# Performance work log

Hardware: AMD Instinct MI355X
Metric: run time of the kernel (lower is better)

Reference implementation:

```python
import jax, jax.numpy as jnp
import numpy as np
import math

FEATURE_DIM = 192  # per-axis dim = 64, n_freqs per axis = 32


def setup_inputs() -> dict:
    key = jax.random.key(0)
    B, N = 4, 65536
    xyz = jax.random.uniform(key, (B, N, 3), dtype=jnp.float32) * 2.0 - 1.0
    d_axis = FEATURE_DIM // 3
    div_term = jnp.exp(
        jnp.arange(0, d_axis, 2, dtype=jnp.float32) * (-math.log(10000.0) / d_axis)
    )  # [nb] = [32], shared by x/y/z axes
    return {"xyz": xyz, "div_term": div_term}


def reference(xyz, div_term):
    # xyz: [B, N, 3], div_term: [nb]
    B, N, _ = xyz.shape
    ang = xyz[..., None] * div_term            # [B, N, 3, nb]
    cos, sin = jnp.cos(ang), jnp.sin(ang)

    def interleave(t):
        # duplicate each frequency into a pair, then interleave axes per bin:
        # per bin i the layout is (x_i, x_i, y_i, y_i, z_i, z_i)
        t2 = jnp.stack([t, t], axis=-1)          # [B, N, 3, nb, 2]
        t2 = jnp.transpose(t2, (0, 1, 3, 2, 4))  # [B, N, nb, 3, 2]
        return t2.reshape(B, N, -1)              # [B, N, 6*nb] = [B, N, feature_dim]

    # position_code: [B, N, feature_dim, 2] with cos at [...,0], sin at [...,1]
    return jnp.stack([interleave(cos), interleave(sin)], axis=-1)
```

## Files before the change

kernel.cpp:

```cpp
#include <hip/hip_runtime.h>


#define UNROLL 8

__global__ __launch_bounds__(256) void rope3d_kernel(
    const float* __restrict__ xyz,
    const float* __restrict__ div_term,
    float4* __restrict__ out,
    int total_f4)
{
    __shared__ float s_div[32];
    if (threadIdx.x < 32) s_div[threadIdx.x] = div_term[threadIdx.x];
    __syncthreads();

    const int stride = blockDim.x * gridDim.x;
    int g = blockIdx.x * blockDim.x + threadIdx.x;

#pragma unroll
    for (int k = 0; k < UNROLL; ++k) {
        if (g < total_f4) {
            unsigned int ug = (unsigned int)g;
            unsigned int p  = ug / 96u;
            unsigned int q  = ug - p * 96u;
            unsigned int bin  = q / 3u;
            unsigned int axis = q - bin * 3u;

            float coord = xyz[p * 3u + axis];
            float ang   = coord * s_div[bin];

            float s, c;
            __sincosf(ang, &s, &c);
            out[g] = make_float4(c, s, c, s);
        }
        g += stride;
    }
}

extern "C" void kernel_launch(void* const* d_in, const int* in_sizes, int n_in,
                              void* d_out, int out_size, void* d_ws, size_t ws_size,
                              hipStream_t stream) {
    const float* xyz      = (const float*)d_in[0];
    const float* div_term = (const float*)d_in[1];
    float*       out      = (float*)d_out;

    int points   = in_sizes[0] / 3;
    int total_f4 = points * 96;

    const int block = 256;
    int grid = (total_f4 + block * UNROLL - 1) / (block * UNROLL);
    rope3d_kernel<<<grid, block, 0, stream>>>(xyz, div_term, (float4*)out, total_f4);
}
```

Baseline: 406.7 us.

## Hoist index math, batch coordinate loads, use nontemporal vector stores

Computes the point/bin/axis decomposition once per thread and relies on the grid being rounded to a multiple of three, so that every later iteration keeps the same bin and axis and only advances the coordinate index by a fixed stride. All coordinates are loaded up front on a fast path before the sincos work, and outputs are written with nontemporal vector stores to cut cache pollution on this write-heavy kernel. The cost is a stride-divisibility assumption: stride/96 must be exact, which holds because the block size of 256 times a multiple of three is divisible by 96. The launch may also add a few extra blocks.

```diff
diff --git a/kernel.cpp b/kernel.cpp
--- a/kernel.cpp
+++ b/kernel.cpp
@@ -3,10 +3,12 @@
 
 #define UNROLL 8
 
+typedef float vfloat4 __attribute__((ext_vector_type(4)));
+
 __global__ __launch_bounds__(256) void rope3d_kernel(
     const float* __restrict__ xyz,
     const float* __restrict__ div_term,
-    float4* __restrict__ out,
+    vfloat4* __restrict__ out,
     int total_f4)
 {
     __shared__ float s_div[32];
@@ -16,23 +18,45 @@
     const int stride = blockDim.x * gridDim.x;
     int g = blockIdx.x * blockDim.x + threadIdx.x;
 
+    unsigned int ug   = (unsigned int)g;
+    unsigned int p    = ug / 96u;
+    unsigned int q    = ug - p * 96u;
+    unsigned int bin  = q / 3u;
+    unsigned int axis = q - bin * 3u;
+
+    const float d       = s_div[bin];
+    const int   cstride = stride >> 5;
+    int         cidx    = (int)(p * 3u + axis);
+
+    if (g + (UNROLL - 1) * stride < total_f4) {
+        float coord[UNROLL];
 #pragma unroll
-    for (int k = 0; k < UNROLL; ++k) {
-        if (g < total_f4) {
-            unsigned int ug = (unsigned int)g;
-            unsigned int p  = ug / 96u;
-            unsigned int q  = ug - p * 96u;
-            unsigned int bin  = q / 3u;
-            unsigned int axis = q - bin * 3u;
-
-            float coord = xyz[p * 3u + axis];
-            float ang   = coord * s_div[bin];
-
-            float s, c;
-            __sincosf(ang, &s, &c);
-            out[g] = make_float4(c, s, c, s);
+        for (int k = 0; k < UNROLL; ++k) {
+            coord[k] = xyz[cidx];
+            cidx += cstride;
         }
-        g += stride;
+#pragma unroll
+        for (int k = 0; k < UNROLL; ++k) {
+            float ang = coord[k] * d;
+            float s = __sinf(ang);
+            float c = __cosf(ang);
+            vfloat4 v = {c, s, c, s};
+            __builtin_nontemporal_store(v, &out[g]);
+            g += stride;
+        }
+    } else {
+#pragma unroll
+        for (int k = 0; k < UNROLL; ++k) {
+            if (g < total_f4) {
+                float ang = xyz[cidx] * d;
+                float s = __sinf(ang);
+                float c = __cosf(ang);
+                vfloat4 v = {c, s, c, s};
+                __builtin_nontemporal_store(v, &out[g]);
+            }
+            cidx += cstride;
+            g += stride;
+        }
     }
 }
 
@@ -48,5 +72,6 @@
 
     const int block = 256;
     int grid = (total_f4 + block * UNROLL - 1) / (block * UNROLL);
-    rope3d_kernel<<<grid, block, 0, stream>>>(xyz, div_term, (float4*)out, total_f4);
+    grid = ((grid + 2) / 3) * 3;
+    rope3d_kernel<<<grid, block, 0, stream>>>(xyz, div_term, (vfloat4*)out, total_f4);
 }
```

New measurement: 398.8 us. Within noise of the previous version (-2.0%).
